# Performance work log

Measured on AMD Instinct MI355X. Metric: run time of the kernel, lower is better.

## Reference

```python
import jax, jax.numpy as jnp
import numpy as np

N_NODES = 50000
N_EDGES = 800000
IN_C = 32
HID = 64
N_LAYERS = 3
EDGE_HID = 128
OUT_C = 1
N_GRAPHS = 8


def setup_inputs() -> dict:
    key = jax.random.key(0)
    ks = jax.random.split(key, 32)
    x = jax.random.normal(ks[0], (N_NODES, IN_C), dtype=jnp.float32)
    # edges with src != dst so that PyG's remove_self_loops is a no-op
    src = jax.random.randint(ks[1], (N_EDGES,), 0, N_NODES)
    off = jax.random.randint(ks[2], (N_EDGES,), 1, N_NODES)
    dst = (src + off) % N_NODES
    edge_index = jnp.stack([src, dst]).astype(jnp.int32)
    batch = jnp.sort(jax.random.randint(ks[3], (N_NODES,), 0, N_GRAPHS)).astype(jnp.int32)
    inp = {"x": x, "edge_index": edge_index, "batch": batch}
    i = 4
    for l in range(N_LAYERS):
        din = IN_C if l == 0 else HID
        s = 1.0 / float(np.sqrt(din))
        inp[f"Wl{l}"] = jax.random.normal(ks[i], (din, HID), dtype=jnp.float32) * s; i += 1
        inp[f"bl{l}"] = jnp.zeros((HID,), jnp.float32)
        inp[f"Wr{l}"] = jax.random.normal(ks[i], (din, HID), dtype=jnp.float32) * s; i += 1
        inp[f"br{l}"] = jnp.zeros((HID,), jnp.float32)
        inp[f"att{l}"] = jax.random.normal(ks[i], (HID,), dtype=jnp.float32) * (1.0 / float(np.sqrt(HID))); i += 1
        inp[f"res{l}"] = jax.random.normal(ks[i], (din, HID), dtype=jnp.float32) * s; i += 1
        inp[f"bias{l}"] = jnp.zeros((HID,), jnp.float32)
        inp[f"lng{l}"] = jnp.ones((HID,), jnp.float32)
        inp[f"lnb{l}"] = jnp.zeros((HID,), jnp.float32)
    efd = 3 * HID
    inp["W1"] = jax.random.normal(ks[i], (efd, EDGE_HID), dtype=jnp.float32) * (1.0 / float(np.sqrt(efd))); i += 1
    inp["b1"] = jnp.zeros((EDGE_HID,), jnp.float32)
    inp["W2"] = jax.random.normal(ks[i], (EDGE_HID, OUT_C), dtype=jnp.float32) * (1.0 / float(np.sqrt(EDGE_HID))); i += 1
    inp["b2"] = jnp.zeros((OUT_C,), jnp.float32)
    return inp


def _gatv2_layer(x, src, dst, Wl, bl, Wr, br, att, resW, bias):
    # GATv2Conv (heads=1, share_weights=False, residual=True, add_self_loops handled by caller)
    n = x.shape[0]
    xl = x @ Wl + bl  # source transform  [N, C]
    xr = x @ Wr + br  # target transform  [N, C]
    e = jax.nn.leaky_relu(xl[src] + xr[dst], 0.2)  # [E, C]
    logits = e @ att                               # [E]
    m = jax.ops.segment_max(logits, dst, num_segments=n)
    ex = jnp.exp(logits - m[dst])
    denom = jax.ops.segment_sum(ex, dst, num_segments=n)
    alpha = ex / denom[dst]                        # edge softmax over incoming edges
    out = jax.ops.segment_sum(alpha[:, None] * xl[src], dst, num_segments=n)
    return out + x @ resW + bias


def _layernorm(h, g, b):
    mu = h.mean(-1, keepdims=True)
    var = h.var(-1, keepdims=True)
    return (h - mu) * jax.lax.rsqrt(var + 1e-5) * g + b


def reference(x, edge_index, batch,
              Wl0, bl0, Wr0, br0, att0, res0, bias0, lng0, lnb0,
              Wl1, bl1, Wr1, br1, att1, res1, bias1, lng1, lnb1,
              Wl2, bl2, Wr2, br2, att2, res2, bias2, lng2, lnb2,
              W1, b1, W2, b2):
    n = x.shape[0]
    loop = jnp.arange(n, dtype=edge_index.dtype)
    src = jnp.concatenate([edge_index[0], loop])  # add self loops
    dst = jnp.concatenate([edge_index[1], loop])
    layers = [(Wl0, bl0, Wr0, br0, att0, res0, bias0, lng0, lnb0),
              (Wl1, bl1, Wr1, br1, att1, res1, bias1, lng1, lnb1),
              (Wl2, bl2, Wr2, br2, att2, res2, bias2, lng2, lnb2)]
    h = x
    for (Wl, bl, Wr, br, att, resW, bias, g, b) in layers:
        h = _gatv2_layer(h, src, dst, Wl, bl, Wr, br, att, resW, bias)
        h = jax.nn.relu(_layernorm(h, g, b))
    node_repr = h
    gc = jax.ops.segment_sum(node_repr, batch, num_segments=N_GRAPHS)  # global_add_pool
    s, d = edge_index[0], edge_index[1]
    edge_feat = jnp.concatenate([node_repr[s], node_repr[d], gc[batch[s]]], axis=-1)  # [E, 3*HID]
    return jax.nn.relu(edge_feat @ W1 + b1) @ W2 + b2
```

## Files before the change

kernel.cpp:

```cpp
#include <hip/hip_runtime.h>
#include <math.h>

typedef float floatx2 __attribute__((ext_vector_type(2)));
typedef float floatx4 __attribute__((ext_vector_type(4)));
typedef short bf16x8 __attribute__((ext_vector_type(8)));
typedef _Float16 halfx2 __attribute__((ext_vector_type(2)));

#define NODE_MASK 0x07FFFFFF
#define LOG2E 1.4426950408889634f

__device__ __forceinline__ float wave_sum(float v){
#pragma unroll
  for (int m = 1; m < 64; m <<= 1) v += __shfl_xor(v, m, 64);
  return v;
}

__device__ __forceinline__ unsigned short bf16_of(float a){
  unsigned ua = __float_as_uint(a);
  ua = (ua + 0x7FFFu + ((ua >> 16) & 1u)) >> 16;
  return (unsigned short)ua;
}
__device__ __forceinline__ unsigned pack_bf16(float a, float b){
  unsigned ua = __float_as_uint(a), ub = __float_as_uint(b);
  ua = (ua + 0x7FFFu + ((ua >> 16) & 1u)) >> 16;
  ub = (ub + 0x7FFFu + ((ub >> 16) & 1u)) >> 16;
  return ua | (ub << 16);
}
__device__ __forceinline__ float2 unpack_bf16(unsigned p){
  float2 r;
  r.x = __uint_as_float(p << 16);
  r.y = __uint_as_float(p & 0xFFFF0000u);
  return r;
}
__device__ __forceinline__ bf16x8 to_bf16x8(float4 a, float4 b){
  bf16x8 r;
  r[0]=(short)bf16_of(a.x); r[1]=(short)bf16_of(a.y);
  r[2]=(short)bf16_of(a.z); r[3]=(short)bf16_of(a.w);
  r[4]=(short)bf16_of(b.x); r[5]=(short)bf16_of(b.y);
  r[6]=(short)bf16_of(b.z); r[7]=(short)bf16_of(b.w);
  return r;
}
__device__ __forceinline__ halfx2 f22h2(float a, float b){
  auto r = __builtin_amdgcn_cvt_pkrtz(a, b);
  return *(halfx2*)&r;
}
__device__ __forceinline__ float fdot2h(halfx2 a, halfx2 b, float c){
  return __builtin_amdgcn_fdot2(a, b, c, false);
}

__global__ __launch_bounds__(256)
void k_deg_t0(const int* __restrict__ dst, int* __restrict__ deg, int* __restrict__ rank, int e,
              const float* __restrict__ h,
              const float* __restrict__ Wl, const float* __restrict__ bl,
              const float* __restrict__ Wr, const float* __restrict__ br,
              const float* __restrict__ Wres, const float* __restrict__ bias,
              unsigned short* __restrict__ xl8, float* __restrict__ xr,
              float* __restrict__ res, int n, int nt64){
  if ((int)blockIdx.x >= nt64){
    int c = blockIdx.x - nt64;
    int i = (c*256 + (int)threadIdx.x)*4;
    if (i + 3 < e){
      int4 d4 = *(const int4*)&dst[i];
      int4 r4;
      r4.x = atomicAdd(&deg[d4.x], 1);
      r4.y = atomicAdd(&deg[d4.y], 1);
      r4.z = atomicAdd(&deg[d4.z], 1);
      r4.w = atomicAdd(&deg[d4.w], 1);
      *(int4*)&rank[i] = r4;
    } else {
      for (int j = i; j < e; ++j) rank[j] = atomicAdd(&deg[dst[j]], 1);
    }
    return;
  }
  const int K = 32, KH = 1;
  int lane = threadIdx.x & 63;
  int nt   = threadIdx.x >> 6;
  int nn = lane & 15, q = lane >> 4;
  int m0 = blockIdx.x * 64;
  if (m0 >= n) return;
  bf16x8 Af[4][KH];
#pragma unroll
  for (int t = 0; t < 4; ++t){
#pragma unroll
    for (int kh = 0; kh < KH; ++kh){
      int node = min(m0 + t*16 + nn, n - 1);
      const float* hp = h + (size_t)node*K + kh*32 + q*8;
      Af[t][kh] = to_bf16x8(*(const float4*)hp, *(const float4*)(hp + 4));
    }
  }
  int n0 = nt * 16;
  for (int sel = 0; sel < 3; ++sel){
    const float* Wp = (sel == 0) ? Wl : (sel == 1) ? Wr : Wres;
    const float* bp = (sel == 0) ? bl : (sel == 1) ? br : bias;
    bf16x8 Bf[KH];
#pragma unroll
    for (int kh = 0; kh < KH; ++kh){
#pragma unroll
      for (int j = 0; j < 8; ++j)
        Bf[kh][j] = (short)bf16_of(Wp[(kh*32 + q*8 + j)*64 + n0 + nn]);
    }
    float bv = bp[n0 + nn];
#pragma unroll
    for (int t = 0; t < 4; ++t){
      floatx4 acc = {bv, bv, bv, bv};
#pragma unroll
      for (int kh = 0; kh < KH; ++kh)
        acc = __builtin_amdgcn_mfma_f32_16x16x32_bf16(Af[t][kh], Bf[kh], acc, 0, 0, 0);
      int nodeb = m0 + t*16 + q*4;
      if (sel == 0){
#pragma unroll
        for (int reg = 0; reg < 4; ++reg){
          float v = acc[reg];
          float p = __shfl_xor(v, 1, 64);
          int node = nodeb + reg;
          if (!(nn & 1) && node < n)
            xl8[(size_t)node*32 + ((n0 + nn) >> 1)] =
              (unsigned short)__builtin_amdgcn_cvt_pk_fp8_f32(v, p, 0, false);
        }
      } else {
        float* op = (sel == 1) ? xr : res;
#pragma unroll
        for (int reg = 0; reg < 4; ++reg){
          int node = nodeb + reg;
          if (node < n) op[(size_t)node*64 + n0 + nn] = acc[reg];
        }
      }
    }
  }
}

__global__ void k_scan_reduce(const int* __restrict__ deg, int* __restrict__ bsum, int n){
  __shared__ int sm[4];
  int i = blockIdx.x*256 + threadIdx.x;
  int v = (i < n) ? (deg[i] + 1) : 0;
#pragma unroll
  for (int m = 1; m < 64; m <<= 1) v += __shfl_xor(v, m, 64);
  if ((threadIdx.x & 63) == 0) sm[threadIdx.x >> 6] = v;
  __syncthreads();
  if (threadIdx.x == 0) bsum[blockIdx.x] = sm[0] + sm[1] + sm[2] + sm[3];
}

__global__ void k_scan_apply(const int* __restrict__ deg, const int* __restrict__ bsum,
                             int* __restrict__ rowptr, int* __restrict__ csr,
                             const int* __restrict__ batch, float* __restrict__ gc,
                             int n, int nb){
  __shared__ int pre[256];
  __shared__ int sm[256];
  int t = threadIdx.x;
  int b = blockIdx.x;
  int pv = (t < nb) ? bsum[t] : 0;
  pre[t] = pv; __syncthreads();
#pragma unroll
  for (int off = 1; off < 256; off <<= 1){
    int x = (t >= off) ? pre[t - off] : 0;
    __syncthreads();
    pre[t] += x;
    __syncthreads();
  }
  int P = (b > 0) ? pre[b - 1] : 0;
  int i = b*256 + t;
  int v = (i < n) ? (deg[i] + 1) : 0;
  sm[t] = v; __syncthreads();
#pragma unroll
  for (int off = 1; off < 256; off <<= 1){
    int x = (t >= off) ? sm[t - off] : 0;
    __syncthreads();
    sm[t] += x;
    __syncthreads();
  }
  if (i < n){
    int r = P + sm[t] - v;
    rowptr[i] = r;
    csr[r] = i | (batch[i] << 27);
  }
  if (b == nb - 1 && t == 255) rowptr[n] = P + sm[255];
  if (b == 0){
    gc[t] = 0.f;
    gc[t + 256] = 0.f;
  }
}

__global__ void k_scatter(const int* __restrict__ src, const int* __restrict__ dst,
                          const int* __restrict__ batch,
                          const int* __restrict__ rowptr, const int* __restrict__ rank,
                          int* __restrict__ csr, int* __restrict__ eidA, int e){
  int i = (blockIdx.x*blockDim.x + threadIdx.x) * 4;
  if (i + 3 < e){
    int4 s4 = *(const int4*)&src[i];
    int4 d4 = *(const int4*)&dst[i];
    int4 r4 = *(const int4*)&rank[i];
    int p0 = rowptr[d4.x] + 1 + r4.x;
    int p1 = rowptr[d4.y] + 1 + r4.y;
    int p2 = rowptr[d4.z] + 1 + r4.z;
    int p3 = rowptr[d4.w] + 1 + r4.w;
    csr[p0] = s4.x | (batch[s4.x] << 27);
    csr[p1] = s4.y | (batch[s4.y] << 27);
    csr[p2] = s4.z | (batch[s4.z] << 27);
    csr[p3] = s4.w | (batch[s4.w] << 27);
    eidA[p0] = i;
    eidA[p1] = i + 1;
    eidA[p2] = i + 2;
    eidA[p3] = i + 3;
  } else {
    for (int j = i; j < e; ++j){
      int d = dst[j], sv = src[j];
      int pos = rowptr[d] + 1 + rank[j];
      csr[pos] = sv | (batch[sv] << 27);
      eidA[pos] = j;
    }
  }
}

template<int K>
__global__ __launch_bounds__(256)
void k_node_transform(const float* __restrict__ h,
                      const float* __restrict__ Wl, const float* __restrict__ bl,
                      const float* __restrict__ Wr, const float* __restrict__ br,
                      const float* __restrict__ Wres, const float* __restrict__ bias,
                      unsigned short* __restrict__ xl8, float* __restrict__ xr,
                      float* __restrict__ res, int n){
  const int KH = K / 32;
  int lane = threadIdx.x & 63;
  int nt   = threadIdx.x >> 6;
  int nn = lane & 15, q = lane >> 4;
  int m0 = blockIdx.x * 64;
  if (m0 >= n) return;
  bf16x8 Af[4][KH];
#pragma unroll
  for (int t = 0; t < 4; ++t){
#pragma unroll
    for (int kh = 0; kh < KH; ++kh){
      int node = min(m0 + t*16 + nn, n - 1);
      const float* hp = h + (size_t)node*K + kh*32 + q*8;
      Af[t][kh] = to_bf16x8(*(const float4*)hp, *(const float4*)(hp + 4));
    }
  }
  int n0 = nt * 16;
  for (int sel = 0; sel < 3; ++sel){
    const float* Wp = (sel == 0) ? Wl : (sel == 1) ? Wr : Wres;
    const float* bp = (sel == 0) ? bl : (sel == 1) ? br : bias;
    bf16x8 Bf[KH];
#pragma unroll
    for (int kh = 0; kh < KH; ++kh){
#pragma unroll
      for (int j = 0; j < 8; ++j)
        Bf[kh][j] = (short)bf16_of(Wp[(kh*32 + q*8 + j)*64 + n0 + nn]);
    }
    float bv = bp[n0 + nn];
#pragma unroll
    for (int t = 0; t < 4; ++t){
      floatx4 acc = {bv, bv, bv, bv};
#pragma unroll
      for (int kh = 0; kh < KH; ++kh)
        acc = __builtin_amdgcn_mfma_f32_16x16x32_bf16(Af[t][kh], Bf[kh], acc, 0, 0, 0);
      int nodeb = m0 + t*16 + q*4;
      if (sel == 0){
#pragma unroll
        for (int reg = 0; reg < 4; ++reg){
          float v = acc[reg];
          float p = __shfl_xor(v, 1, 64);
          int node = nodeb + reg;
          if (!(nn & 1) && node < n)
            xl8[(size_t)node*32 + ((n0 + nn) >> 1)] =
              (unsigned short)__builtin_amdgcn_cvt_pk_fp8_f32(v, p, 0, false);
        }
      } else {
        float* op = (sel == 1) ? xr : res;
#pragma unroll
        for (int reg = 0; reg < 4; ++reg){
          int node = nodeb + reg;
          if (node < n) op[(size_t)node*64 + n0 + nn] = acc[reg];
        }
      }
    }
  }
}

__global__ void k_gat_edge(const uint2* __restrict__ xl_u2, const float* __restrict__ xr,
                           const float* __restrict__ att,
                           const float* __restrict__ lng, const float* __restrict__ lnb,
                           const int* __restrict__ rowptr, const int* __restrict__ csr,
                           float* __restrict__ hio, int n){
  int node = (blockIdx.x*blockDim.x + threadIdx.x) >> 6;
  int lane = threadIdx.x & 63;
  if (node >= n) return;
  int sub = lane >> 3;
  int l   = lane & 7;
  size_t base = (size_t)node*64 + 8*l;
  float4 xr0 = *(const float4*)&xr[base];
  float4 xr1 = *(const float4*)&xr[base + 4];
  float4 at0f = *(const float4*)&att[8*l];
  float4 at1f = *(const float4*)&att[8*l + 4];
  halfx2 xh0 = f22h2(xr0.x, xr0.y), xh1 = f22h2(xr0.z, xr0.w);
  halfx2 xh2 = f22h2(xr1.x, xr1.y), xh3 = f22h2(xr1.z, xr1.w);
  halfx2 at0 = f22h2(at0f.x*LOG2E, at0f.y*LOG2E);
  halfx2 at1 = f22h2(at0f.z*LOG2E, at0f.w*LOG2E);
  halfx2 at2 = f22h2(at1f.x*LOG2E, at1f.y*LOG2E);
  halfx2 at3 = f22h2(at1f.z*LOG2E, at1f.w*LOG2E);
  halfx2 z2  = {(_Float16)0.f, (_Float16)0.f};
  halfx2 c02 = {(_Float16)0.2f, (_Float16)0.2f};
  int p0 = rowptr[node], p1 = rowptr[node+1];
  int deg = p1 - p0;
  int sreg = csr[p0 + min(lane, deg-1)];
  int rounds = (deg + 7) >> 3;
  float dsum = 0.f;
  float a0=0.f,a1=0.f,a2=0.f,a3=0.f,a4=0.f,a5=0.f,a6=0.f,a7=0.f;
  int e0 = sub;
  bool v0 = e0 < deg;
  int s0 = __shfl(sreg, v0 ? e0 : 0, 64) & NODE_MASK;
  uint2 x0 = xl_u2[(size_t)s0*8 + l];
  int e1 = 8 + sub;
  bool v1 = e1 < deg;
  uint2 x1 = x0;
  if (rounds > 1){
    int s1 = __shfl(sreg, v1 ? e1 : 0, 64) & NODE_MASK;
    x1 = xl_u2[(size_t)s1*8 + l];
  }
  for (int r = 0; r < rounds; ++r){
    int en = 8*(r+2) + sub;
    bool vn = en < deg;
    uint2 xn = x0;
    if (r + 2 < rounds){
      int sn;
      if (en < 64) sn = __shfl(sreg, vn ? en : 0, 64);
      else         sn = csr[p0 + (vn ? en : 0)];
      sn &= NODE_MASK;
      xn = xl_u2[(size_t)sn*8 + l];
    }
    floatx2 p01 = __builtin_amdgcn_cvt_pk_f32_fp8(x0.x, false);
    floatx2 p23 = __builtin_amdgcn_cvt_pk_f32_fp8(x0.x, true);
    floatx2 p45 = __builtin_amdgcn_cvt_pk_f32_fp8(x0.y, false);
    floatx2 p67 = __builtin_amdgcn_cvt_pk_f32_fp8(x0.y, true);
    halfx2 v0h = f22h2(p01.x, p01.y) + xh0;
    halfx2 v1h = f22h2(p23.x, p23.y) + xh1;
    halfx2 v2h = f22h2(p45.x, p45.y) + xh2;
    halfx2 v3h = f22h2(p67.x, p67.y) + xh3;
    halfx2 lr0 = __builtin_elementwise_min(v0h, z2) * c02 + __builtin_elementwise_max(v0h, z2);
    halfx2 lr1 = __builtin_elementwise_min(v1h, z2) * c02 + __builtin_elementwise_max(v1h, z2);
    halfx2 lr2 = __builtin_elementwise_min(v2h, z2) * c02 + __builtin_elementwise_max(v2h, z2);
    halfx2 lr3 = __builtin_elementwise_min(v3h, z2) * c02 + __builtin_elementwise_max(v3h, z2);
    float partial = fdot2h(lr3, at3, fdot2h(lr2, at2, fdot2h(lr1, at1, fdot2h(lr0, at0, 0.f))));
#pragma unroll
    for (int mm = 1; mm < 8; mm <<= 1) partial += __shfl_xor(partial, mm, 64);
    float w = v0 ? exp2f(partial) : 0.f;
    dsum += w;
    a0 = fmaf(w, p01.x, a0);
    a1 = fmaf(w, p01.y, a1);
    a2 = fmaf(w, p23.x, a2);
    a3 = fmaf(w, p23.y, a3);
    a4 = fmaf(w, p45.x, a4);
    a5 = fmaf(w, p45.y, a5);
    a6 = fmaf(w, p67.x, a6);
    a7 = fmaf(w, p67.y, a7);
    x0 = x1; v0 = v1;
    x1 = xn; v1 = vn;
  }
#pragma unroll
  for (int off = 8; off < 64; off <<= 1){
    dsum += __shfl_xor(dsum, off, 64);
    a0 += __shfl_xor(a0, off, 64);
    a1 += __shfl_xor(a1, off, 64);
    a2 += __shfl_xor(a2, off, 64);
    a3 += __shfl_xor(a3, off, 64);
    a4 += __shfl_xor(a4, off, 64);
    a5 += __shfl_xor(a5, off, 64);
    a6 += __shfl_xor(a6, off, 64);
    a7 += __shfl_xor(a7, off, 64);
  }
  float4 r0 = *(const float4*)&hio[base];
  float4 r1 = *(const float4*)&hio[base + 4];
  float inv = __builtin_amdgcn_rcpf(dsum);
  float o0 = fmaf(a0, inv, r0.x);
  float o1 = fmaf(a1, inv, r0.y);
  float o2 = fmaf(a2, inv, r0.z);
  float o3 = fmaf(a3, inv, r0.w);
  float o4 = fmaf(a4, inv, r1.x);
  float o5 = fmaf(a5, inv, r1.y);
  float o6 = fmaf(a6, inv, r1.z);
  float o7 = fmaf(a7, inv, r1.w);
  float mean = wave_sum(o0+o1+o2+o3+o4+o5+o6+o7) * (1.f/512.f);
  float d0 = o0-mean, d1 = o1-mean, d2 = o2-mean, d3 = o3-mean;
  float d4 = o4-mean, d5 = o5-mean, d6 = o6-mean, d7 = o7-mean;
  float var = wave_sum(d0*d0+d1*d1+d2*d2+d3*d3+d4*d4+d5*d5+d6*d6+d7*d7) * (1.f/512.f);
  float rstd = rsqrtf(var + 1e-5f);
  if (sub == 0){
    float4 lg0 = *(const float4*)&lng[8*l];
    float4 lg1 = *(const float4*)&lng[8*l + 4];
    float4 lb0 = *(const float4*)&lnb[8*l];
    float4 lb1 = *(const float4*)&lnb[8*l + 4];
    float4 out0, out1;
    out0.x = fmaxf(fmaf(d0*rstd, lg0.x, lb0.x), 0.f);
    out0.y = fmaxf(fmaf(d1*rstd, lg0.y, lb0.y), 0.f);
    out0.z = fmaxf(fmaf(d2*rstd, lg0.z, lb0.z), 0.f);
    out0.w = fmaxf(fmaf(d3*rstd, lg0.w, lb0.w), 0.f);
    out1.x = fmaxf(fmaf(d4*rstd, lg1.x, lb1.x), 0.f);
    out1.y = fmaxf(fmaf(d5*rstd, lg1.y, lb1.y), 0.f);
    out1.z = fmaxf(fmaf(d6*rstd, lg1.z, lb1.z), 0.f);
    out1.w = fmaxf(fmaf(d7*rstd, lg1.w, lb1.w), 0.f);
    *(float4*)&hio[base] = out0;
    *(float4*)&hio[base + 4] = out1;
  }
}

__global__ void k_graph_proj(const float* __restrict__ gc, const float* __restrict__ W1,
                             const float* __restrict__ b1, unsigned* __restrict__ Gh){
  int g = blockIdx.x;
  int j = threadIdx.x;
  float a = b1[j];
#pragma unroll 8
  for (int k = 0; k < 64; ++k) a = fmaf(gc[g*64+k], W1[(128+k)*128 + j], a);
  float p = __shfl_xor(a, 1, 64);
  if (!(j & 1)){
    halfx2 hv = f22h2(a, p);
    Gh[g*64 + (j >> 1)] = *(unsigned*)&hv;
  }
}

__global__ __launch_bounds__(256)
void k_node_proj_pool(const float* __restrict__ nr, const float* __restrict__ W1,
                      const int* __restrict__ batch,
                      unsigned short* __restrict__ Au16, unsigned* __restrict__ Bu,
                      float* __restrict__ gc, int n, int nt64){
  int lane = threadIdx.x & 63;
  int wave = threadIdx.x >> 6;
  if ((int)blockIdx.x >= nt64){
    int wid = (blockIdx.x - nt64)*4 + wave;
    int n0 = wid*64;
    if (n0 >= n) return;
    int n1 = min(n0 + 64, n);
    int last = n1 - 1 - n0;
    int bt = batch[min(n0 + lane, n - 1)];
    int curg = __shfl(bt, 0, 64);
    float s = 0.f;
#pragma unroll
    for (int bb = 0; bb < 64; bb += 8){
      if (bb > last) break;
      float v0_ = (bb+0 <= last) ? nr[(size_t)(n0+bb+0)*64 + lane] : 0.f;
      float v1_ = (bb+1 <= last) ? nr[(size_t)(n0+bb+1)*64 + lane] : 0.f;
      float v2_ = (bb+2 <= last) ? nr[(size_t)(n0+bb+2)*64 + lane] : 0.f;
      float v3_ = (bb+3 <= last) ? nr[(size_t)(n0+bb+3)*64 + lane] : 0.f;
      float v4_ = (bb+4 <= last) ? nr[(size_t)(n0+bb+4)*64 + lane] : 0.f;
      float v5_ = (bb+5 <= last) ? nr[(size_t)(n0+bb+5)*64 + lane] : 0.f;
      float v6_ = (bb+6 <= last) ? nr[(size_t)(n0+bb+6)*64 + lane] : 0.f;
      float v7_ = (bb+7 <= last) ? nr[(size_t)(n0+bb+7)*64 + lane] : 0.f;
#pragma unroll
      for (int j = 0; j < 8; ++j){
        int g = __shfl(bt, min(bb + j, last), 64);
        if (g != curg){ atomicAdd(&gc[curg*64 + lane], s); s = 0.f; curg = g; }
        float vj = (j==0)?v0_:(j==1)?v1_:(j==2)?v2_:(j==3)?v3_:
                   (j==4)?v4_:(j==5)?v5_:(j==6)?v6_:v7_;
        s += vj;
      }
    }
    atomicAdd(&gc[curg*64 + lane], s);
    return;
  }
  int nn = lane & 15, q = lane >> 4;
  int m0 = blockIdx.x * 64;
  bf16x8 Af[4][2];
#pragma unroll
  for (int t = 0; t < 4; ++t){
#pragma unroll
    for (int kh = 0; kh < 2; ++kh){
      int node = min(m0 + t*16 + nn, n - 1);
      const float* hp = nr + (size_t)node*64 + kh*32 + q*8;
      Af[t][kh] = to_bf16x8(*(const float4*)hp, *(const float4*)(hp + 4));
    }
  }
  for (int half = 0; half < 2; ++half){
#pragma unroll
    for (int ni = 0; ni < 2; ++ni){
      int nt = wave + ni*4;
      int n0 = nt * 16;
      bf16x8 Bf[2];
#pragma unroll
      for (int kh = 0; kh < 2; ++kh){
#pragma unroll
        for (int j = 0; j < 8; ++j)
          Bf[kh][j] = (short)bf16_of(W1[(half*64 + kh*32 + q*8 + j)*128 + n0 + nn]);
      }
#pragma unroll
      for (int t = 0; t < 4; ++t){
        floatx4 acc = {0.f, 0.f, 0.f, 0.f};
#pragma unroll
        for (int kh = 0; kh < 2; ++kh)
          acc = __builtin_amdgcn_mfma_f32_16x16x32_bf16(Af[t][kh], Bf[kh], acc, 0, 0, 0);
        int nodeb = m0 + t*16 + q*4;
#pragma unroll
        for (int reg = 0; reg < 4; ++reg){
          float v = acc[reg];
          float p = __shfl_xor(v, 1, 64);
          int node = nodeb + reg;
          if (!(nn & 1) && node < n){
            int j = (n0 + nn) >> 1;
            if (half == 0)
              Au16[(size_t)node*64 + j] =
                (unsigned short)__builtin_amdgcn_cvt_pk_fp8_f32(v, p, 0, false);
            else
              Bu[(size_t)node*64 + j] = pack_bf16(v, p);
          }
        }
      }
    }
  }
}

__global__ void k_edge_out_csr(const uint4* __restrict__ Au4, const uint4* __restrict__ Bu4,
                               const unsigned* __restrict__ Gh,
                               const int* __restrict__ rowptr, const int* __restrict__ csr,
                               const int* __restrict__ eidA,
                               const float* __restrict__ W2, const float* __restrict__ b2,
                               float* __restrict__ out, int n){
  int node = (blockIdx.x*blockDim.x + threadIdx.x) >> 6;
  int lane = threadIdx.x & 63;
  if (node >= n) return;
  int sub = lane >> 3;
  int l   = lane & 7;
  int p0 = rowptr[node];
  int deg2 = rowptr[node+1] - p0 - 1;
  if (deg2 <= 0) return;
  int idx = p0 + 1 + min(lane, deg2-1);
  int sreg = csr[idx];
  int ereg = eidA[idx];
  uint4 ba = Bu4[(size_t)node*16 + 2*l];
  uint4 bb = Bu4[(size_t)node*16 + 2*l + 1];
  float2 t0 = unpack_bf16(ba.x), t1 = unpack_bf16(ba.y);
  float2 t2 = unpack_bf16(ba.z), t3 = unpack_bf16(ba.w);
  float2 t4 = unpack_bf16(bb.x), t5 = unpack_bf16(bb.y);
  float2 t6 = unpack_bf16(bb.z), t7 = unpack_bf16(bb.w);
  halfx2 bh0 = f22h2(t0.x, t0.y), bh1 = f22h2(t1.x, t1.y);
  halfx2 bh2 = f22h2(t2.x, t2.y), bh3 = f22h2(t3.x, t3.y);
  halfx2 bh4 = f22h2(t4.x, t4.y), bh5 = f22h2(t5.x, t5.y);
  halfx2 bh6 = f22h2(t6.x, t6.y), bh7 = f22h2(t7.x, t7.y);
  float4 w0 = *(const float4*)&W2[16*l];
  float4 w1 = *(const float4*)&W2[16*l + 4];
  float4 w2 = *(const float4*)&W2[16*l + 8];
  float4 w3 = *(const float4*)&W2[16*l + 12];
  halfx2 wh0 = f22h2(w0.x, w0.y), wh1 = f22h2(w0.z, w0.w);
  halfx2 wh2 = f22h2(w1.x, w1.y), wh3 = f22h2(w1.z, w1.w);
  halfx2 wh4 = f22h2(w2.x, w2.y), wh5 = f22h2(w2.z, w2.w);
  halfx2 wh6 = f22h2(w3.x, w3.y), wh7 = f22h2(w3.z, w3.w);
  halfx2 z2 = {(_Float16)0.f, (_Float16)0.f};
  float b2v = b2[0];
  int rounds = (deg2 + 7) >> 3;
  int e0 = sub;
  bool v0 = e0 < deg2;
  int q0 = v0 ? e0 : 0;
  int c0 = __shfl(sreg, q0, 64);
  int id0 = __shfl(ereg, q0, 64);
  uint4 A0 = Au4[(size_t)(c0 & NODE_MASK)*8 + l];
  int e1 = 8 + sub;
  bool v1 = e1 < deg2;
  int c1 = c0, id1 = id0; uint4 A1 = A0;
  if (rounds > 1){
    int q1 = v1 ? e1 : 0;
    c1 = __shfl(sreg, q1, 64);
    id1 = __shfl(ereg, q1, 64);
    A1 = Au4[(size_t)(c1 & NODE_MASK)*8 + l];
  }
  for (int r = 0; r < rounds; ++r){
    int en = 8*(r+2) + sub;
    bool vn = en < deg2;
    int cn = c0, idn = id0; uint4 An = A0;
    if (r + 2 < rounds){
      int qn = vn ? en : 0;
      if (en < 64){ cn = __shfl(sreg, qn, 64); idn = __shfl(ereg, qn, 64); }
      else        { cn = csr[p0 + 1 + qn];     idn = eidA[p0 + 1 + qn]; }
      An = Au4[(size_t)(cn & NODE_MASK)*8 + l];
    }
    int g = ((unsigned)c0) >> 27;
    const uint4* gp = (const uint4*)(Gh + g*64 + 8*l);
    uint4 g0 = gp[0], g1 = gp[1];
    halfx2 gh0 = *(halfx2*)&g0.x, gh1 = *(halfx2*)&g0.y;
    halfx2 gh2 = *(halfx2*)&g0.z, gh3 = *(halfx2*)&g0.w;
    halfx2 gh4 = *(halfx2*)&g1.x, gh5 = *(halfx2*)&g1.y;
    halfx2 gh6 = *(halfx2*)&g1.z, gh7 = *(halfx2*)&g1.w;
    floatx2 a01 = __builtin_amdgcn_cvt_pk_f32_fp8(A0.x, false);
    floatx2 a23 = __builtin_amdgcn_cvt_pk_f32_fp8(A0.x, true);
    floatx2 a45 = __builtin_amdgcn_cvt_pk_f32_fp8(A0.y, false);
    floatx2 a67 = __builtin_amdgcn_cvt_pk_f32_fp8(A0.y, true);
    floatx2 a89 = __builtin_amdgcn_cvt_pk_f32_fp8(A0.z, false);
    floatx2 aab = __builtin_amdgcn_cvt_pk_f32_fp8(A0.z, true);
    floatx2 acd = __builtin_amdgcn_cvt_pk_f32_fp8(A0.w, false);
    floatx2 aef = __builtin_amdgcn_cvt_pk_f32_fp8(A0.w, true);
    halfx2 h0 = __builtin_elementwise_max(f22h2(a01.x, a01.y) + bh0 + gh0, z2);
    halfx2 h1 = __builtin_elementwise_max(f22h2(a23.x, a23.y) + bh1 + gh1, z2);
    halfx2 h2 = __builtin_elementwise_max(f22h2(a45.x, a45.y) + bh2 + gh2, z2);
    halfx2 h3 = __builtin_elementwise_max(f22h2(a67.x, a67.y) + bh3 + gh3, z2);
    halfx2 h4 = __builtin_elementwise_max(f22h2(a89.x, a89.y) + bh4 + gh4, z2);
    halfx2 h5 = __builtin_elementwise_max(f22h2(aab.x, aab.y) + bh5 + gh5, z2);
    halfx2 h6 = __builtin_elementwise_max(f22h2(acd.x, acd.y) + bh6 + gh6, z2);
    halfx2 h7 = __builtin_elementwise_max(f22h2(aef.x, aef.y) + bh7 + gh7, z2);
    float part = fdot2h(h7, wh7, fdot2h(h6, wh6, fdot2h(h5, wh5, fdot2h(h4, wh4,
                 fdot2h(h3, wh3, fdot2h(h2, wh2, fdot2h(h1, wh1, fdot2h(h0, wh0, 0.f))))))));
#pragma unroll
    for (int mm = 1; mm < 8; mm <<= 1) part += __shfl_xor(part, mm, 64);
    if (l == 0 && v0) out[id0] = part + b2v;
    c0 = c1; id0 = id1; A0 = A1; v0 = v1;
    c1 = cn; id1 = idn; A1 = An; v1 = vn;
  }
}

extern "C" void kernel_launch(void* const* d_in, const int* in_sizes, int n_in,
                              void* d_out, int out_size, void* d_ws, size_t ws_size,
                              hipStream_t stream){
  const float* x     = (const float*)d_in[0];
  const int*   ei    = (const int*)d_in[1];
  const int*   batch = (const int*)d_in[2];
  const int N = in_sizes[2];
  const int E = in_sizes[1] / 2;
  const int* src = ei;
  const int* dst = ei + E;

  unsigned* W = (unsigned*)d_ws;
  const size_t N16 = (size_t)N * 16;
  const size_t N32 = (size_t)N * 32;
  const size_t N64 = (size_t)N * 64;
  unsigned short* xl8 = (unsigned short*)W;
  float* xr = (float*)(W + N16);
  float* hE = (float*)(W + N16 + N64);
  float* hD = (float*)(W + N16 + 2*N64);
  unsigned short* Au16 = (unsigned short*)W;
  unsigned* Bu = W + N32;
  int* rowptr = (int*)(W + N16 + 3*N64);
  int* deg    = rowptr + (N + 16);
  int* csr    = deg + N;
  int* rank   = csr + (N + E);
  int* eidA   = rank + E;
  float* gc   = (float*)(eidA + (N + E));
  unsigned* Gh = (unsigned*)(gc + 512);
  int* bsum   = (int*)(Gh + 512);

  const int NB = (N + 255) / 256;
  const int NT64 = (N + 63) / 64;
  const int ECH = (E/4 + 255) / 256;

  (void)hipMemsetAsync(deg, 0, (size_t)N*4, stream);
  const float* Wl0   = (const float*)d_in[3];
  const float* bl0   = (const float*)d_in[4];
  const float* Wr0   = (const float*)d_in[5];
  const float* br0   = (const float*)d_in[6];
  const float* Wres0 = (const float*)d_in[8];
  const float* bias0 = (const float*)d_in[9];
  k_deg_t0 <<<NT64 + ECH, 256, 0, stream>>>(dst, deg, rank, E,
                                            x, Wl0, bl0, Wr0, br0, Wres0, bias0,
                                            xl8, xr, hD, N, NT64);
  k_scan_reduce<<<NB, 256, 0, stream>>>(deg, bsum, N);
  k_scan_apply <<<NB, 256, 0, stream>>>(deg, bsum, rowptr, csr, batch, gc, N, NB);
  k_scatter    <<<ECH, 256, 0, stream>>>(src, dst, batch, rowptr, rank, csr, eidA, E);

  const float* h = hD;
  float* hn = hD;
  for (int l = 0; l < 3; ++l){
    const float* Wl   = (const float*)d_in[3 + 9*l + 0];
    const float* bl   = (const float*)d_in[3 + 9*l + 1];
    const float* Wr   = (const float*)d_in[3 + 9*l + 2];
    const float* br   = (const float*)d_in[3 + 9*l + 3];
    const float* att  = (const float*)d_in[3 + 9*l + 4];
    const float* Wres = (const float*)d_in[3 + 9*l + 5];
    const float* bias = (const float*)d_in[3 + 9*l + 6];
    const float* lng  = (const float*)d_in[3 + 9*l + 7];
    const float* lnb  = (const float*)d_in[3 + 9*l + 8];
    if (l > 0)
      k_node_transform<64><<<NT64, 256, 0, stream>>>(h, Wl, bl, Wr, br, Wres, bias, xl8, xr, hn, N);
    k_gat_edge<<<(N+3)/4, 256, 0, stream>>>((const uint2*)xl8, xr, att, lng, lnb, rowptr, csr, hn, N);
    h = hn;
    hn = (l == 0) ? hE : hD;
  }

  const float* W1 = (const float*)d_in[30];
  const float* b1 = (const float*)d_in[31];
  const float* W2 = (const float*)d_in[32];
  const float* b2 = (const float*)d_in[33];

  int pool_waves = (N + 63) / 64;
  int poolB = (pool_waves + 3) / 4;
  k_node_proj_pool<<<NT64 + poolB, 256, 0, stream>>>(hD, W1, batch, Au16, Bu, gc, N, NT64);
  k_graph_proj<<<8, 128, 0, stream>>>(gc, W1, b1, Gh);
  k_edge_out_csr<<<(N+3)/4, 256, 0, stream>>>((const uint4*)Au16, (const uint4*)Bu, Gh,
                                              rowptr, csr, eidA, W2, b2, (float*)d_out, N);
}
```

Measured before the change: 392.6 us.

## Pad degree counters, interleave CSR source and edge id, hoist residual load

Degree counters are spaced 16 ints apart (one per 64-byte line) so the atomics in the degree pass do not fight over shared cache lines. The separate csr and eidA arrays become one int2 array, so the output kernel gets the source and edge id from a single 8-byte load. The attention kernel now issues its residual load at the start so it overlaps with the edge loop. In exchange the degree buffer and memset are 16x larger, and the attention kernel reads 8-byte entries where it needs only 4 bytes, doubling its CSR traffic.

New measurement: 379.5 us (median of 2 runs). 1.03x faster.

```diff
diff --git a/kernel.cpp b/kernel.cpp
--- a/kernel.cpp
+++ b/kernel.cpp
@@ -8,6 +8,7 @@
 
 #define NODE_MASK 0x07FFFFFF
 #define LOG2E 1.4426950408889634f
+#define DEG_STRIDE 16
 
 __device__ __forceinline__ float wave_sum(float v){
 #pragma unroll
@@ -49,7 +50,7 @@
 }
 
 __global__ __launch_bounds__(256)
-void k_deg_t0(const int* __restrict__ dst, int* __restrict__ deg, int* __restrict__ rank, int e,
+void k_deg_t0(const int* __restrict__ dst, int* __restrict__ deg16, int* __restrict__ rank, int e,
               const float* __restrict__ h,
               const float* __restrict__ Wl, const float* __restrict__ bl,
               const float* __restrict__ Wr, const float* __restrict__ br,
@@ -62,13 +63,13 @@
     if (i + 3 < e){
       int4 d4 = *(const int4*)&dst[i];
       int4 r4;
-      r4.x = atomicAdd(&deg[d4.x], 1);
-      r4.y = atomicAdd(&deg[d4.y], 1);
-      r4.z = atomicAdd(&deg[d4.z], 1);
-      r4.w = atomicAdd(&deg[d4.w], 1);
+      r4.x = atomicAdd(&deg16[d4.x*DEG_STRIDE], 1);
+      r4.y = atomicAdd(&deg16[d4.y*DEG_STRIDE], 1);
+      r4.z = atomicAdd(&deg16[d4.z*DEG_STRIDE], 1);
+      r4.w = atomicAdd(&deg16[d4.w*DEG_STRIDE], 1);
       *(int4*)&rank[i] = r4;
     } else {
-      for (int j = i; j < e; ++j) rank[j] = atomicAdd(&deg[dst[j]], 1);
+      for (int j = i; j < e; ++j) rank[j] = atomicAdd(&deg16[dst[j]*DEG_STRIDE], 1);
     }
     return;
   }
@@ -129,10 +130,10 @@
   }
 }
 
-__global__ void k_scan_reduce(const int* __restrict__ deg, int* __restrict__ bsum, int n){
+__global__ void k_scan_reduce(const int* __restrict__ deg16, int* __restrict__ bsum, int n){
   __shared__ int sm[4];
   int i = blockIdx.x*256 + threadIdx.x;
-  int v = (i < n) ? (deg[i] + 1) : 0;
+  int v = (i < n) ? (deg16[i*DEG_STRIDE] + 1) : 0;
 #pragma unroll
   for (int m = 1; m < 64; m <<= 1) v += __shfl_xor(v, m, 64);
   if ((threadIdx.x & 63) == 0) sm[threadIdx.x >> 6] = v;
@@ -140,8 +141,8 @@
   if (threadIdx.x == 0) bsum[blockIdx.x] = sm[0] + sm[1] + sm[2] + sm[3];
 }
 
-__global__ void k_scan_apply(const int* __restrict__ deg, const int* __restrict__ bsum,
-                             int* __restrict__ rowptr, int* __restrict__ csr,
+__global__ void k_scan_apply(const int* __restrict__ deg16, const int* __restrict__ bsum,
+                             int* __restrict__ rowptr, int2* __restrict__ cs2,
                              const int* __restrict__ batch, float* __restrict__ gc,
                              int n, int nb){
   __shared__ int pre[256];
@@ -159,7 +160,7 @@
   }
   int P = (b > 0) ? pre[b - 1] : 0;
   int i = b*256 + t;
-  int v = (i < n) ? (deg[i] + 1) : 0;
+  int v = (i < n) ? (deg16[i*DEG_STRIDE] + 1) : 0;
   sm[t] = v; __syncthreads();
 #pragma unroll
   for (int off = 1; off < 256; off <<= 1){
@@ -171,7 +172,7 @@
   if (i < n){
     int r = P + sm[t] - v;
     rowptr[i] = r;
-    csr[r] = i | (batch[i] << 27);
+    cs2[r] = make_int2(i | (batch[i] << 27), 0);
   }
   if (b == nb - 1 && t == 255) rowptr[n] = P + sm[255];
   if (b == 0){
@@ -183,7 +184,7 @@
 __global__ void k_scatter(const int* __restrict__ src, const int* __restrict__ dst,
                           const int* __restrict__ batch,
                           const int* __restrict__ rowptr, const int* __restrict__ rank,
-                          int* __restrict__ csr, int* __restrict__ eidA, int e){
+                          int2* __restrict__ cs2, int e){
   int i = (blockIdx.x*blockDim.x + threadIdx.x) * 4;
   if (i + 3 < e){
     int4 s4 = *(const int4*)&src[i];
@@ -193,20 +194,15 @@
     int p1 = rowptr[d4.y] + 1 + r4.y;
     int p2 = rowptr[d4.z] + 1 + r4.z;
     int p3 = rowptr[d4.w] + 1 + r4.w;
-    csr[p0] = s4.x | (batch[s4.x] << 27);
-    csr[p1] = s4.y | (batch[s4.y] << 27);
-    csr[p2] = s4.z | (batch[s4.z] << 27);
-    csr[p3] = s4.w | (batch[s4.w] << 27);
-    eidA[p0] = i;
-    eidA[p1] = i + 1;
-    eidA[p2] = i + 2;
-    eidA[p3] = i + 3;
+    cs2[p0] = make_int2(s4.x | (batch[s4.x] << 27), i);
+    cs2[p1] = make_int2(s4.y | (batch[s4.y] << 27), i + 1);
+    cs2[p2] = make_int2(s4.z | (batch[s4.z] << 27), i + 2);
+    cs2[p3] = make_int2(s4.w | (batch[s4.w] << 27), i + 3);
   } else {
     for (int j = i; j < e; ++j){
       int d = dst[j], sv = src[j];
       int pos = rowptr[d] + 1 + rank[j];
-      csr[pos] = sv | (batch[sv] << 27);
-      eidA[pos] = j;
+      cs2[pos] = make_int2(sv | (batch[sv] << 27), j);
     }
   }
 }
@@ -279,7 +275,7 @@
 __global__ void k_gat_edge(const uint2* __restrict__ xl_u2, const float* __restrict__ xr,
                            const float* __restrict__ att,
                            const float* __restrict__ lng, const float* __restrict__ lnb,
-                           const int* __restrict__ rowptr, const int* __restrict__ csr,
+                           const int* __restrict__ rowptr, const int2* __restrict__ cs2,
                            float* __restrict__ hio, int n){
   int node = (blockIdx.x*blockDim.x + threadIdx.x) >> 6;
   int lane = threadIdx.x & 63;
@@ -287,6 +283,8 @@
   int sub = lane >> 3;
   int l   = lane & 7;
   size_t base = (size_t)node*64 + 8*l;
+  float4 r0 = *(const float4*)&hio[base];
+  float4 r1 = *(const float4*)&hio[base + 4];
   float4 xr0 = *(const float4*)&xr[base];
   float4 xr1 = *(const float4*)&xr[base + 4];
   float4 at0f = *(const float4*)&att[8*l];
@@ -301,7 +299,7 @@
   halfx2 c02 = {(_Float16)0.2f, (_Float16)0.2f};
   int p0 = rowptr[node], p1 = rowptr[node+1];
   int deg = p1 - p0;
-  int sreg = csr[p0 + min(lane, deg-1)];
+  int sreg = cs2[p0 + min(lane, deg-1)].x;
   int rounds = (deg + 7) >> 3;
   float dsum = 0.f;
   float a0=0.f,a1=0.f,a2=0.f,a3=0.f,a4=0.f,a5=0.f,a6=0.f,a7=0.f;
@@ -323,7 +321,7 @@
     if (r + 2 < rounds){
       int sn;
       if (en < 64) sn = __shfl(sreg, vn ? en : 0, 64);
-      else         sn = csr[p0 + (vn ? en : 0)];
+      else         sn = cs2[p0 + (vn ? en : 0)].x;
       sn &= NODE_MASK;
       xn = xl_u2[(size_t)sn*8 + l];
     }
@@ -367,8 +365,6 @@
     a6 += __shfl_xor(a6, off, 64);
     a7 += __shfl_xor(a7, off, 64);
   }
-  float4 r0 = *(const float4*)&hio[base];
-  float4 r1 = *(const float4*)&hio[base + 4];
   float inv = __builtin_amdgcn_rcpf(dsum);
   float o0 = fmaf(a0, inv, r0.x);
   float o1 = fmaf(a1, inv, r0.y);
@@ -507,8 +503,7 @@
 
 __global__ void k_edge_out_csr(const uint4* __restrict__ Au4, const uint4* __restrict__ Bu4,
                                const unsigned* __restrict__ Gh,
-                               const int* __restrict__ rowptr, const int* __restrict__ csr,
-                               const int* __restrict__ eidA,
+                               const int* __restrict__ rowptr, const int2* __restrict__ cs2,
                                const float* __restrict__ W2, const float* __restrict__ b2,
                                float* __restrict__ out, int n){
   int node = (blockIdx.x*blockDim.x + threadIdx.x) >> 6;
@@ -519,9 +514,9 @@
   int p0 = rowptr[node];
   int deg2 = rowptr[node+1] - p0 - 1;
   if (deg2 <= 0) return;
-  int idx = p0 + 1 + min(lane, deg2-1);
-  int sreg = csr[idx];
-  int ereg = eidA[idx];
+  int2 slot = cs2[p0 + 1 + min(lane, deg2-1)];
+  int sreg = slot.x;
+  int ereg = slot.y;
   uint4 ba = Bu4[(size_t)node*16 + 2*l];
   uint4 bb = Bu4[(size_t)node*16 + 2*l + 1];
   float2 t0 = unpack_bf16(ba.x), t1 = unpack_bf16(ba.y);
@@ -565,7 +560,7 @@
     if (r + 2 < rounds){
       int qn = vn ? en : 0;
       if (en < 64){ cn = __shfl(sreg, qn, 64); idn = __shfl(ereg, qn, 64); }
-      else        { cn = csr[p0 + 1 + qn];     idn = eidA[p0 + 1 + qn]; }
+      else        { int2 sv = cs2[p0 + 1 + qn]; cn = sv.x; idn = sv.y; }
       An = Au4[(size_t)(cn & NODE_MASK)*8 + l];
     }
     int g = ((unsigned)c0) >> 27;
@@ -623,11 +618,10 @@
   unsigned short* Au16 = (unsigned short*)W;
   unsigned* Bu = W + N32;
   int* rowptr = (int*)(W + N16 + 3*N64);
-  int* deg    = rowptr + (N + 16);
-  int* csr    = deg + N;
-  int* rank   = csr + (N + E);
-  int* eidA   = rank + E;
-  float* gc   = (float*)(eidA + (N + E));
+  int* deg16  = rowptr + (N + 16);
+  int2* cs2   = (int2*)(deg16 + (size_t)16*N);
+  int* rank   = (int*)(cs2 + (N + E));
+  float* gc   = (float*)(rank + E);
   unsigned* Gh = (unsigned*)(gc + 512);
   int* bsum   = (int*)(Gh + 512);
 
@@ -635,19 +629,19 @@
   const int NT64 = (N + 63) / 64;
   const int ECH = (E/4 + 255) / 256;
 
-  (void)hipMemsetAsync(deg, 0, (size_t)N*4, stream);
+  (void)hipMemsetAsync(deg16, 0, (size_t)N*16*4, stream);
   const float* Wl0   = (const float*)d_in[3];
   const float* bl0   = (const float*)d_in[4];
   const float* Wr0   = (const float*)d_in[5];
   const float* br0   = (const float*)d_in[6];
   const float* Wres0 = (const float*)d_in[8];
   const float* bias0 = (const float*)d_in[9];
-  k_deg_t0 <<<NT64 + ECH, 256, 0, stream>>>(dst, deg, rank, E,
+  k_deg_t0 <<<NT64 + ECH, 256, 0, stream>>>(dst, deg16, rank, E,
                                             x, Wl0, bl0, Wr0, br0, Wres0, bias0,
                                             xl8, xr, hD, N, NT64);
-  k_scan_reduce<<<NB, 256, 0, stream>>>(deg, bsum, N);
-  k_scan_apply <<<NB, 256, 0, stream>>>(deg, bsum, rowptr, csr, batch, gc, N, NB);
-  k_scatter    <<<ECH, 256, 0, stream>>>(src, dst, batch, rowptr, rank, csr, eidA, E);
+  k_scan_reduce<<<NB, 256, 0, stream>>>(deg16, bsum, N);
+  k_scan_apply <<<NB, 256, 0, stream>>>(deg16, bsum, rowptr, cs2, batch, gc, N, NB);
+  k_scatter    <<<ECH, 256, 0, stream>>>(src, dst, batch, rowptr, rank, cs2, E);
 
   const float* h = hD;
   float* hn = hD;
@@ -663,7 +657,7 @@
     const float* lnb  = (const float*)d_in[3 + 9*l + 8];
     if (l > 0)
       k_node_transform<64><<<NT64, 256, 0, stream>>>(h, Wl, bl, Wr, br, Wres, bias, xl8, xr, hn, N);
-    k_gat_edge<<<(N+3)/4, 256, 0, stream>>>((const uint2*)xl8, xr, att, lng, lnb, rowptr, csr, hn, N);
+    k_gat_edge<<<(N+3)/4, 256, 0, stream>>>((const uint2*)xl8, xr, att, lng, lnb, rowptr, cs2, hn, N);
     h = hn;
     hn = (l == 0) ? hE : hD;
   }
@@ -678,5 +672,5 @@
   k_node_proj_pool<<<NT64 + poolB, 256, 0, stream>>>(hD, W1, batch, Au16, Bu, gc, N, NT64);
   k_graph_proj<<<8, 128, 0, stream>>>(gc, W1, b1, Gh);
   k_edge_out_csr<<<(N+3)/4, 256, 0, stream>>>((const uint4*)Au16, (const uint4*)Bu, Gh,
-                                              rowptr, csr, eidA, W2, b2, (float*)d_out, N);
-}
+                                              rowptr, cs2, W2, b2, (float*)d_out, N);
+}
```
